# Performance work log

Hardware: AMD Instinct MI355X
Metric: run time of the kernel (lower is better)

The kernel has to match this reference:

```python
import jax, jax.numpy as jnp
import numpy as np

N = 50000      # nodes
E = 800000     # edges
D_IN = 128
D_H = 256
D_OUT = 128
EPS = 1e-5
SLOPE = 0.01   # LeakyReLU negative_slope


def setup_inputs() -> dict:
    key = jax.random.key(0)
    ks = jax.random.split(key, 24)
    inp = {}
    inp["x"] = jax.random.normal(ks[0], (N, D_IN), dtype=jnp.float32)
    inp["edge_index"] = jax.random.randint(ks[1], (2, E), 0, N, dtype=jnp.int32)
    dims = [(D_IN, D_H), (D_H, D_H), (D_H, D_H), (D_H, D_OUT)]
    for i, (di, do) in enumerate(dims, start=1):
        inp[f"W{i}"] = jax.random.normal(ks[4 * i - 2], (di, do), dtype=jnp.float32) / np.float32(np.sqrt(di))
        inp[f"b{i}"] = jnp.zeros((do,), dtype=jnp.float32)
        inp[f"g{i}"] = 1.0 + 0.1 * jax.random.normal(ks[4 * i - 1], (do,), dtype=jnp.float32)   # BN gamma
        inp[f"be{i}"] = 0.1 * jax.random.normal(ks[4 * i], (do,), dtype=jnp.float32)            # BN beta
    inp["ln_g"] = 1.0 + 0.1 * jax.random.normal(ks[18], (D_OUT,), dtype=jnp.float32)
    inp["ln_b"] = 0.1 * jax.random.normal(ks[19], (D_OUT,), dtype=jnp.float32)
    return inp


def _gcn_conv(x, W, b, src, dst, nisq):
    # PyG GCNConv: linear first, then sym-normalized aggregation with self-loops.
    xl = x @ W                                   # [N, do]
    coef = (nisq[src] * nisq[dst])[:, None]      # [E, 1]
    msg = xl[src] * coef                         # [E, do] gather
    agg = jax.ops.segment_sum(msg, dst, num_segments=N)  # scatter-add
    # self-loop contribution: deg^{-1/2}_i * deg^{-1/2}_i * xl_i
    return agg + xl * (nisq * nisq)[:, None] + b


def _bn(x, g, b):
    # BatchNorm1d, training-mode batch statistics (biased variance)
    m = jnp.mean(x, axis=0)
    v = jnp.var(x, axis=0)
    return (x - m) * jax.lax.rsqrt(v + EPS) * g + b


def _lrelu(x):
    return jnp.where(x >= 0, x, SLOPE * x)


def _layer_norm(x, g, b):
    m = jnp.mean(x, axis=-1, keepdims=True)
    v = jnp.var(x, axis=-1, keepdims=True)
    return (x - m) * jax.lax.rsqrt(v + EPS) * g + b


def reference(x, edge_index, W1, b1, g1, be1, W2, b2, g2, be2, W3, b3, g3, be3, W4, b4, g4, be4, ln_g, ln_b):
    src = edge_index[0]
    dst = edge_index[1]
    # degrees with self-loops (computed once, shared by all 4 convs)
    deg = jax.ops.segment_sum(jnp.ones((E,), dtype=x.dtype), dst, num_segments=N) + 1.0
    nisq = jax.lax.rsqrt(deg)  # deg >= 1 so safe

    identity = x  # input_dim == output_dim -> residual_fc is Identity
    h = _lrelu(_bn(_gcn_conv(x, W1, b1, src, dst, nisq), g1, be1))   # dropout = identity (eval)
    h = _lrelu(_bn(_gcn_conv(h, W2, b2, src, dst, nisq), g2, be2))
    h = _lrelu(_bn(_gcn_conv(h, W3, b3, src, dst, nisq), g3, be3))
    h = _gcn_conv(h, W4, b4, src, dst, nisq)
    h = h + identity
    return _layer_norm(_bn(h, g4, be4), ln_g, ln_b)
```

## Files before the change

### kernel.cpp

```cpp
#include <hip/hip_runtime.h>

#define N_NODES 50000
#define NPAD 50176
#define N_EDGES 800000
#define EPS_C 1e-5f
#define SLOPE_C 0.01f

typedef __attribute__((ext_vector_type(8))) short short8v;
typedef __attribute__((ext_vector_type(4))) float f32x4;

__device__ __forceinline__ unsigned short f2bf(float f) {
  unsigned u = __float_as_uint(f);
  u += 0x7fffu + ((u >> 16) & 1u);
  return (unsigned short)(u >> 16);
}
__device__ __forceinline__ unsigned packbf(float a, float b) {
  return (unsigned)f2bf(a) | ((unsigned)f2bf(b) << 16);
}
__device__ __forceinline__ float bflo(unsigned u) { return __uint_as_float(u << 16); }
__device__ __forceinline__ float bfhi(unsigned u) { return __uint_as_float(u & 0xffff0000u); }

__device__ __forceinline__ void gload16(const unsigned short* g, unsigned short* l) {
  __builtin_amdgcn_global_load_lds(
      (const __attribute__((address_space(1))) unsigned int*)g,
      (__attribute__((address_space(3))) unsigned int*)l, 16, 0, 0);
}

__global__ void wcast_all_kernel(const float* __restrict__ W1, const float* __restrict__ W2,
                                 const float* __restrict__ W3, const float* __restrict__ W4,
                                 unsigned short* __restrict__ Wt1, unsigned short* __restrict__ Wt2,
                                 unsigned short* __restrict__ Wt3, unsigned short* __restrict__ Wt4) {
  const int y = blockIdx.y;
  const int idx = blockIdx.x * 256 + threadIdx.x;
  const float* W;
  unsigned short* Wt;
  int K, mshift, mmask, total;
  switch (y) {
    case 0: W = W1; Wt = Wt1; K = 128; mshift = 8; mmask = 255; total = 32768; break;
    case 1: W = W2; Wt = Wt2; K = 256; mshift = 8; mmask = 255; total = 65536; break;
    case 2: W = W3; Wt = Wt3; K = 256; mshift = 8; mmask = 255; total = 65536; break;
    default: W = W4; Wt = Wt4; K = 256; mshift = 7; mmask = 127; total = 32768; break;
  }
  if (idx >= total) return;
  const int k = idx >> mshift;
  const int m = idx & mmask;
  Wt[(size_t)m * K + k] = f2bf(W[idx]);
}

template <int MODE, int KC>
__global__ __launch_bounds__(256) void gemm2_kernel(
    const unsigned short* __restrict__ A, const unsigned short* __restrict__ Wt,
    const float* __restrict__ bias, unsigned short* __restrict__ Yb,
    float* __restrict__ colsum, float* __restrict__ colsumsq, int M) {
  __shared__ __align__(16) unsigned short Bs[64][KC];
  __shared__ __align__(16) unsigned short As[128][64];
  __shared__ float sred[2][64][2];
  const int tid = threadIdx.x;
  const int lane = tid & 63;
  const int wave = tid >> 6;
  const int wr = wave >> 1, wc = wave & 1;
  const int row0 = blockIdx.x * 128;
  const int col0 = blockIdx.y * 64;
  const int l15 = lane & 15;
  const int lhi = lane >> 4;

  constexpr int CPR = KC / 8;
  constexpr int BITER = 64 * CPR / 256;
#pragma unroll
  for (int c = 0; c < BITER; ++c) {
    const int ch = c * 256 + tid;
    const int rb = ch / CPR;
    const int cb = ch % CPR;
    const short8v v =
        *reinterpret_cast<const short8v*>(&Wt[(size_t)(col0 + rb) * KC + cb * 8]);
    *reinterpret_cast<short8v*>(&Bs[rb][(cb ^ (rb & 7)) * 8]) = v;
  }

  f32x4 acc[4][2];
#pragma unroll
  for (int i = 0; i < 4; ++i)
#pragma unroll
    for (int j = 0; j < 2; ++j) acc[i][j] = (f32x4){0.f, 0.f, 0.f, 0.f};

  for (int k0 = 0; k0 < KC; k0 += 64) {
    __syncthreads();
#pragma unroll
    for (int c = 0; c < 4; ++c) {
      const int chunk = (c * 4 + wave) * 64 + lane;
      const int r = chunk >> 3;
      const int cksrc = (chunk & 7) ^ (r & 7);
      gload16(&A[(size_t)(row0 + r) * KC + k0 + cksrc * 8], &As[0][0] + chunk * 8);
    }
    __syncthreads();
    short8v bfr[2][2];
#pragma unroll
    for (int nr = 0; nr < 2; ++nr)
#pragma unroll
      for (int h = 0; h < 2; ++h) {
        const int rowb = wc * 32 + nr * 16 + l15;
        const int chb = (k0 >> 3) + h * 4 + lhi;
        bfr[nr][h] = *reinterpret_cast<const short8v*>(&Bs[rowb][(chb ^ (rowb & 7)) * 8]);
      }
#pragma unroll
    for (int mr = 0; mr < 4; ++mr) {
#pragma unroll
      for (int h = 0; h < 2; ++h) {
        const int rowa = wr * 64 + mr * 16 + l15;
        const int cha = (h * 4 + lhi) ^ (rowa & 7);
        const short8v af = *reinterpret_cast<const short8v*>(&As[rowa][cha * 8]);
#pragma unroll
        for (int nr = 0; nr < 2; ++nr)
          acc[mr][nr] = __builtin_amdgcn_mfma_f32_16x16x32_bf16(
              af, bfr[nr][h], acc[mr][nr], 0, 0, 0);
      }
    }
  }
  float bcol[2] = {0.f, 0.f};
  if constexpr (MODE == 1) {
#pragma unroll
    for (int nr = 0; nr < 2; ++nr) bcol[nr] = bias[col0 + wc * 32 + nr * 16 + l15];
  }
  float s_c[2] = {0.f, 0.f}, q_c[2] = {0.f, 0.f};
#pragma unroll
  for (int mr = 0; mr < 4; ++mr) {
#pragma unroll
    for (int r = 0; r < 4; ++r) {
      const int grow = row0 + wr * 64 + mr * 16 + lhi * 4 + r;
#pragma unroll
      for (int nr = 0; nr < 2; ++nr) {
        const int gcol = col0 + wc * 32 + nr * 16 + l15;
        const float v = acc[mr][nr][r] + bcol[nr];
        Yb[(size_t)grow * M + gcol] = f2bf(v);
        if constexpr (MODE == 1) {
          if (grow < N_NODES) {
            s_c[nr] += v;
            q_c[nr] += v * v;
          }
        }
      }
    }
  }
  if constexpr (MODE == 1) {
#pragma unroll
    for (int nr = 0; nr < 2; ++nr) {
      float s = s_c[nr], q = q_c[nr];
      s += __shfl_xor(s, 16, 64); q += __shfl_xor(q, 16, 64);
      s += __shfl_xor(s, 32, 64); q += __shfl_xor(q, 32, 64);
      if (lhi == 0) {
        const int cl = wc * 32 + nr * 16 + l15;
        sred[0][cl][wr] = s;
        sred[1][cl][wr] = q;
      }
    }
    __syncthreads();
    if (tid < 128) {
      const int which = tid >> 6;
      const int cl = tid & 63;
      const float tot = sred[which][cl][0] + sred[which][cl][1];
      float* dstp = which ? colsumsq : colsum;
      atomicAdd(&dstp[col0 + cl], tot);
    }
  }
}

__global__ void hist_kernel(const int* __restrict__ dst, int* __restrict__ hist, int E) {
  const int e = blockIdx.x * 256 + threadIdx.x;
  if (e < E) atomicAdd(&hist[dst[e]], 1);
}

__global__ __launch_bounds__(1024) void scan1_kernel(
    const int* __restrict__ hist, int* __restrict__ off, int* __restrict__ partial,
    float* __restrict__ nisq, int n) {
  __shared__ int tmp[1024];
  const int tid = threadIdx.x;
  const int i = blockIdx.x * 1024 + tid;
  const int v = (i < n) ? hist[i] : 0;
  tmp[tid] = v;
  __syncthreads();
  int x = v;
  for (int o = 1; o < 1024; o <<= 1) {
    const int y = (tid >= o) ? tmp[tid - o] : 0;
    __syncthreads();
    x += y;
    tmp[tid] = x;
    __syncthreads();
  }
  if (i < n) {
    off[i] = x - v;
    nisq[i] = rsqrtf((float)v + 1.0f);
  }
  if (tid == 1023) partial[blockIdx.x] = x;
}

__global__ __launch_bounds__(64) void scan2_kernel(
    const int* __restrict__ partial, int* __restrict__ partialoff,
    int* __restrict__ offN, int nb) {
  const int tid = threadIdx.x;
  const int v = (tid < nb) ? partial[tid] : 0;
  int x = v;
  for (int o = 1; o < 64; o <<= 1) {
    const int y = __shfl_up(x, o, 64);
    if (tid >= o) x += y;
  }
  if (tid < nb) partialoff[tid] = x - v;
  if (tid == 63) *offN = x;
}

__global__ void scan3_kernel(int* __restrict__ off, int* __restrict__ cursor,
                             const int* __restrict__ partialoff, int n) {
  const int i = blockIdx.x * 256 + threadIdx.x;
  if (i < n) {
    const int o = off[i] + partialoff[i >> 10];
    off[i] = o;
    cursor[i] = o;
  }
}

__global__ void scatter_kernel(const int* __restrict__ src, const int* __restrict__ dst,
                               int* __restrict__ cursor, int* __restrict__ esorted, int E) {
  const int e = blockIdx.x * 256 + threadIdx.x;
  if (e < E) {
    const int p = atomicAdd(&cursor[dst[e]], 1);
    esorted[p] = src[e];
  }
}

__global__ void scale_cast_kernel(const float* __restrict__ x,
                                  const float* __restrict__ nisq,
                                  unsigned short* __restrict__ xs) {
  const int idx = blockIdx.x * 256 + threadIdx.x;
  if (idx >= N_NODES * 32) return;
  const int row = idx >> 5;
  const int c = (idx & 31) * 4;
  const float s = nisq[row];
  const float4 v = *reinterpret_cast<const float4*>(&x[(size_t)row * 128 + c]);
  ushort4 o;
  o.x = f2bf(v.x * s); o.y = f2bf(v.y * s);
  o.z = f2bf(v.z * s); o.w = f2bf(v.w * s);
  *reinterpret_cast<ushort4*>(&xs[(size_t)row * 128 + c]) = o;
}

template <int DO, bool ADD_BIAS, bool HAS_RES, bool OUT_BF16>
__global__ __launch_bounds__(256) void aggregate4_kernel(
    const unsigned short* __restrict__ Y, const int* __restrict__ segoff,
    const int* __restrict__ esorted, const float* __restrict__ nisq,
    const float* __restrict__ bias, const float* __restrict__ resid,
    void* __restrict__ Tv) {
  constexpr int V2 = DO / 32;
  const int wave = threadIdx.x >> 6;
  const int lane = threadIdx.x & 63;
  const int half = lane >> 5;
  const int l31 = lane & 31;
  const int n = blockIdx.x * 4 + wave;
  const int colbase = l31 * V2;
  if (n >= N_NODES) {
    if (half == 0) {
      if constexpr (OUT_BF16) {
        unsigned short* tr = (unsigned short*)Tv + (size_t)n * DO + colbase;
        if constexpr (V2 == 8) *reinterpret_cast<uint4*>(tr) = (uint4){0, 0, 0, 0};
        else *reinterpret_cast<uint2*>(tr) = (uint2){0, 0};
      } else {
        float* tr = (float*)Tv + (size_t)n * DO + colbase;
        if constexpr (V2 == 8) {
          *reinterpret_cast<float4*>(tr) = (float4){0.f, 0.f, 0.f, 0.f};
          *reinterpret_cast<float4*>(tr + 4) = (float4){0.f, 0.f, 0.f, 0.f};
        } else {
          *reinterpret_cast<float4*>(tr) = (float4){0.f, 0.f, 0.f, 0.f};
        }
      }
    }
    return;
  }
  const unsigned short* Yc = Y + colbase;
  float a0[V2], a1[V2];
#pragma unroll
  for (int i = 0; i < V2; ++i) { a0[i] = 0.f; a1[i] = 0.f; }
  const int s = segoff[n];
  const int e = segoff[n + 1];

  if constexpr (V2 == 8) {
    auto acc8 = [&](float* a, const uint4 v) {
      a[0] += bflo(v.x); a[1] += bfhi(v.x);
      a[2] += bflo(v.y); a[3] += bfhi(v.y);
      a[4] += bflo(v.z); a[5] += bfhi(v.z);
      a[6] += bflo(v.w); a[7] += bfhi(v.w);
    };
    int j = s + half;
    for (; j + 2 < e; j += 4) {
      const int i0 = esorted[j];
      const int i1 = esorted[j + 2];
      const uint4 v0 = *reinterpret_cast<const uint4*>(Yc + (size_t)i0 * DO);
      const uint4 v1 = *reinterpret_cast<const uint4*>(Yc + (size_t)i1 * DO);
      acc8(a0, v0); acc8(a1, v1);
    }
    if (j < e) acc8(a0, *reinterpret_cast<const uint4*>(Yc + (size_t)esorted[j] * DO));
    if (half == 0) acc8(a1, *reinterpret_cast<const uint4*>(Yc + (size_t)n * DO));
  } else {
    auto acc4 = [&](float* a, const uint2 v) {
      a[0] += bflo(v.x); a[1] += bfhi(v.x);
      a[2] += bflo(v.y); a[3] += bfhi(v.y);
    };
    int j = s + half;
    for (; j + 2 < e; j += 4) {
      const int i0 = esorted[j];
      const int i1 = esorted[j + 2];
      const uint2 v0 = *reinterpret_cast<const uint2*>(Yc + (size_t)i0 * DO);
      const uint2 v1 = *reinterpret_cast<const uint2*>(Yc + (size_t)i1 * DO);
      acc4(a0, v0); acc4(a1, v1);
    }
    if (j < e) acc4(a0, *reinterpret_cast<const uint2*>(Yc + (size_t)esorted[j] * DO));
    if (half == 0) acc4(a1, *reinterpret_cast<const uint2*>(Yc + (size_t)n * DO));
  }

  const float sc = nisq[n];
  float vals[V2];
#pragma unroll
  for (int i = 0; i < V2; ++i) {
    float t = a0[i] + a1[i];
    t += __shfl_xor(t, 32, 64);
    t *= sc;
    if (half == 0) {
      if (ADD_BIAS) t += bias[colbase + i];
      if (HAS_RES) t += resid[(size_t)n * DO + colbase + i];
    }
    vals[i] = t;
  }
  if (half == 0) {
    if constexpr (OUT_BF16) {
      unsigned short* tr = (unsigned short*)Tv + (size_t)n * DO + colbase;
      if constexpr (V2 == 8) {
        uint4 o;
        o.x = packbf(vals[0], vals[1]); o.y = packbf(vals[2], vals[3]);
        o.z = packbf(vals[4], vals[5]); o.w = packbf(vals[6], vals[7]);
        *reinterpret_cast<uint4*>(tr) = o;
      } else {
        uint2 o;
        o.x = packbf(vals[0], vals[1]); o.y = packbf(vals[2], vals[3]);
        *reinterpret_cast<uint2*>(tr) = o;
      }
    } else {
      float* tr = (float*)Tv + (size_t)n * DO + colbase;
      if constexpr (V2 == 8) {
        float4 o0 = {vals[0], vals[1], vals[2], vals[3]};
        float4 o1 = {vals[4], vals[5], vals[6], vals[7]};
        *reinterpret_cast<float4*>(tr) = o0;
        *reinterpret_cast<float4*>(tr + 4) = o1;
      } else {
        float4 o = {vals[0], vals[1], vals[2], vals[3]};
        *reinterpret_cast<float4*>(tr) = o;
      }
    }
  }
}

__global__ void stats_kernel(const float* __restrict__ T, float* __restrict__ colsum,
                             float* __restrict__ colsumsq, int n, int rowsPerBlock) {
  const int c = threadIdx.x;
  const int DO = blockDim.x;
  const int r0 = blockIdx.x * rowsPerBlock;
  int r1 = r0 + rowsPerBlock;
  if (r1 > n) r1 = n;
  float s = 0.f, q = 0.f;
  for (int r = r0; r < r1; ++r) {
    const float v = T[(size_t)r * DO + c];
    s += v;
    q += v * v;
  }
  atomicAdd(&colsum[c], s);
  atomicAdd(&colsumsq[c], q);
}

__global__ void bn_lrelu_nisq_kernel(const unsigned short* __restrict__ Tb,
                                     const float* __restrict__ colsum,
                                     const float* __restrict__ colsumsq,
                                     const float* __restrict__ g, const float* __restrict__ be,
                                     const float* __restrict__ nisq,
                                     unsigned short* __restrict__ outb,
                                     size_t total8, float invN) {
  const size_t idx = (size_t)blockIdx.x * 256 + threadIdx.x;
  if (idx >= total8) return;
  const int row = (int)(idx >> 5);
  if (row >= N_NODES) {
    *reinterpret_cast<uint4*>(&outb[idx * 8]) = (uint4){0, 0, 0, 0};
    return;
  }
  const unsigned c = ((unsigned)idx & 31u) * 8;
  const float sc = nisq[row];
  uint4 v = *reinterpret_cast<const uint4*>(&Tb[idx * 8]);
  float z[8] = {bflo(v.x), bfhi(v.x), bflo(v.y), bfhi(v.y),
                bflo(v.z), bfhi(v.z), bflo(v.w), bfhi(v.w)};
  const float4 cs0 = *reinterpret_cast<const float4*>(&colsum[c]);
  const float4 cs1 = *reinterpret_cast<const float4*>(&colsum[c + 4]);
  const float4 cq0 = *reinterpret_cast<const float4*>(&colsumsq[c]);
  const float4 cq1 = *reinterpret_cast<const float4*>(&colsumsq[c + 4]);
  const float4 gv0 = *reinterpret_cast<const float4*>(&g[c]);
  const float4 gv1 = *reinterpret_cast<const float4*>(&g[c + 4]);
  const float4 bv0 = *reinterpret_cast<const float4*>(&be[c]);
  const float4 bv1 = *reinterpret_cast<const float4*>(&be[c + 4]);
  const float css[8] = {cs0.x, cs0.y, cs0.z, cs0.w, cs1.x, cs1.y, cs1.z, cs1.w};
  const float cqq[8] = {cq0.x, cq0.y, cq0.z, cq0.w, cq1.x, cq1.y, cq1.z, cq1.w};
  const float ggg[8] = {gv0.x, gv0.y, gv0.z, gv0.w, gv1.x, gv1.y, gv1.z, gv1.w};
  const float bbb[8] = {bv0.x, bv0.y, bv0.z, bv0.w, bv1.x, bv1.y, bv1.z, bv1.w};
#pragma unroll
  for (int k = 0; k < 8; ++k) {
    const float m = css[k] * invN;
    const float rs = rsqrtf(cqq[k] * invN - m * m + EPS_C);
    float zz = (z[k] - m) * rs * ggg[k] + bbb[k];
    zz = (zz >= 0.f) ? zz : SLOPE_C * zz;
    z[k] = zz * sc;
  }
  v.x = packbf(z[0], z[1]); v.y = packbf(z[2], z[3]);
  v.z = packbf(z[4], z[5]); v.w = packbf(z[6], z[7]);
  *reinterpret_cast<uint4*>(&outb[idx * 8]) = v;
}

__global__ __launch_bounds__(256) void bn_ln_kernel(
    const float* __restrict__ T, const float* __restrict__ colsum,
    const float* __restrict__ colsumsq, const float* __restrict__ g,
    const float* __restrict__ be, const float* __restrict__ lng,
    const float* __restrict__ lnb, float* __restrict__ out, float invN) {
  const int wave = threadIdx.x >> 6;
  const int lane = threadIdx.x & 63;
  const int n = blockIdx.x * 4 + wave;
  if (n >= N_NODES) return;
  const int c = lane * 2;
  const float2 t = *reinterpret_cast<const float2*>(&T[(size_t)n * 128 + c]);
  float z[2];
#pragma unroll
  for (int k = 0; k < 2; ++k) {
    const float m = colsum[c + k] * invN;
    const float v = colsumsq[c + k] * invN - m * m;
    const float tv = (k == 0) ? t.x : t.y;
    z[k] = (tv - m) * rsqrtf(v + EPS_C) * g[c + k] + be[c + k];
  }
  float s = z[0] + z[1];
  float q = z[0] * z[0] + z[1] * z[1];
  for (int o = 32; o > 0; o >>= 1) {
    s += __shfl_xor(s, o, 64);
    q += __shfl_xor(q, o, 64);
  }
  const float mean = s * (1.f / 128.f);
  const float var = q * (1.f / 128.f) - mean * mean;
  const float rs = rsqrtf(var + EPS_C);
  float2 o2;
  o2.x = (z[0] - mean) * rs * lng[c] + lnb[c];
  o2.y = (z[1] - mean) * rs * lng[c + 1] + lnb[c + 1];
  *reinterpret_cast<float2*>(&out[(size_t)n * 128 + c]) = o2;
}

extern "C" void kernel_launch(void* const* d_in, const int* in_sizes, int n_in,
                              void* d_out, int out_size, void* d_ws, size_t ws_size,
                              hipStream_t stream) {
  const float* x = (const float*)d_in[0];
  const int* ei = (const int*)d_in[1];
  const int* srcp = ei;
  const int* dstp = ei + N_EDGES;
  const float* W1 = (const float*)d_in[2];
  const float* b1 = (const float*)d_in[3];
  const float* g1 = (const float*)d_in[4];
  const float* be1 = (const float*)d_in[5];
  const float* W2 = (const float*)d_in[6];
  const float* b2 = (const float*)d_in[7];
  const float* g2 = (const float*)d_in[8];
  const float* be2 = (const float*)d_in[9];
  const float* W3 = (const float*)d_in[10];
  const float* b3 = (const float*)d_in[11];
  const float* g3 = (const float*)d_in[12];
  const float* be3 = (const float*)d_in[13];
  const float* W4 = (const float*)d_in[14];
  const float* b4 = (const float*)d_in[15];
  const float* g4 = (const float*)d_in[16];
  const float* be4 = (const float*)d_in[17];
  const float* lng = (const float*)d_in[18];
  const float* lnb = (const float*)d_in[19];
  float* out = (float*)d_out;

  char* ws = (char*)d_ws;
  size_t off_b = 0;
  auto alloc = [&](size_t bytes) -> void* {
    void* p = (void*)(ws + off_b);
    off_b += (bytes + 255) & ~(size_t)255;
    return p;
  };
  int* hist = (int*)alloc((size_t)N_NODES * 4);
  float* cs1 = (float*)alloc(256 * 4);
  float* cq1 = (float*)alloc(256 * 4);
  float* cs2 = (float*)alloc(256 * 4);
  float* cq2 = (float*)alloc(256 * 4);
  float* cs3 = (float*)alloc(256 * 4);
  float* cq3 = (float*)alloc(256 * 4);
  float* cs4 = (float*)alloc(256 * 4);
  float* cq4 = (float*)alloc(256 * 4);
  const size_t zero_bytes = off_b;
  int* segoff = (int*)alloc((size_t)(N_NODES + 1) * 4);
  int* cursor = (int*)alloc((size_t)N_NODES * 4);
  float* nisq = (float*)alloc((size_t)N_NODES * 4);
  int* esorted = (int*)alloc((size_t)N_EDGES * 4);
  int* partial = (int*)alloc(64 * 4);
  int* partialoff = (int*)alloc(64 * 4);
  unsigned short* Wt1 = (unsigned short*)alloc((size_t)256 * 128 * 2);
  unsigned short* Wt2 = (unsigned short*)alloc((size_t)256 * 256 * 2);
  unsigned short* Wt3 = (unsigned short*)alloc((size_t)256 * 256 * 2);
  unsigned short* Wt4 = (unsigned short*)alloc((size_t)128 * 256 * 2);
  unsigned short* tblA = (unsigned short*)alloc((size_t)NPAD * 256 * 2);
  unsigned short* tblB = (unsigned short*)alloc((size_t)NPAD * 256 * 2);
  unsigned short* S = (unsigned short*)alloc((size_t)NPAD * 256 * 2);
  unsigned short* Tb = (unsigned short*)alloc((size_t)NPAD * 256 * 2);
  float* Tf = (float*)alloc((size_t)NPAD * 128 * 4);

  const float invN = 1.0f / (float)N_NODES;
  const int egrid = (N_EDGES + 255) / 256;
  const int ngrid = (N_NODES + 255) / 256;
  const int aggrid = NPAD / 4;
  const int statgrid = (N_NODES + 127) / 128;
  const int nb = (N_NODES + 1023) / 1024;
  const dim3 mgrid256(NPAD / 128, 4);
  const dim3 mgrid128(NPAD / 128, 2);
  const unsigned bngrid = (unsigned)(((size_t)NPAD * 32 + 255) / 256);

  hipMemsetAsync(hist, 0, zero_bytes, stream);

  hist_kernel<<<egrid, 256, 0, stream>>>(dstp, hist, N_EDGES);
  scan1_kernel<<<nb, 1024, 0, stream>>>(hist, segoff, partial, nisq, N_NODES);
  scan2_kernel<<<1, 64, 0, stream>>>(partial, partialoff, &segoff[N_NODES], nb);
  scan3_kernel<<<ngrid, 256, 0, stream>>>(segoff, cursor, partialoff, N_NODES);
  scatter_kernel<<<egrid, 256, 0, stream>>>(srcp, dstp, cursor, esorted, N_EDGES);

  wcast_all_kernel<<<dim3(256, 4), 256, 0, stream>>>(W1, W2, W3, W4, Wt1, Wt2, Wt3, Wt4);

  scale_cast_kernel<<<(N_NODES * 32 + 255) / 256, 256, 0, stream>>>(x, nisq, tblA);
  aggregate4_kernel<128, false, false, true><<<aggrid, 256, 0, stream>>>(
      tblA, segoff, esorted, nisq, nullptr, nullptr, S);
  gemm2_kernel<1, 128><<<mgrid256, 256, 0, stream>>>(S, Wt1, b1, Tb, cs1, cq1, 256);
  bn_lrelu_nisq_kernel<<<bngrid, 256, 0, stream>>>(Tb, cs1, cq1, g1, be1, nisq,
                                                   tblB, (size_t)NPAD * 32, invN);

  aggregate4_kernel<256, false, false, true><<<aggrid, 256, 0, stream>>>(
      tblB, segoff, esorted, nisq, nullptr, nullptr, S);
  gemm2_kernel<1, 256><<<mgrid256, 256, 0, stream>>>(S, Wt2, b2, Tb, cs2, cq2, 256);
  bn_lrelu_nisq_kernel<<<bngrid, 256, 0, stream>>>(Tb, cs2, cq2, g2, be2, nisq,
                                                   tblA, (size_t)NPAD * 32, invN);

  aggregate4_kernel<256, false, false, true><<<aggrid, 256, 0, stream>>>(
      tblA, segoff, esorted, nisq, nullptr, nullptr, S);
  gemm2_kernel<1, 256><<<mgrid256, 256, 0, stream>>>(S, Wt3, b3, Tb, cs3, cq3, 256);
  bn_lrelu_nisq_kernel<<<bngrid, 256, 0, stream>>>(Tb, cs3, cq3, g3, be3, nisq,
                                                   tblB, (size_t)NPAD * 32, invN);

  gemm2_kernel<0, 256><<<mgrid128, 256, 0, stream>>>(tblB, Wt4, nullptr, S, nullptr, nullptr, 128);
  aggregate4_kernel<128, true, true, false><<<aggrid, 256, 0, stream>>>(
      S, segoff, esorted, nisq, b4, x, Tf);
  stats_kernel<<<statgrid, 128, 0, stream>>>(Tf, cs4, cq4, N_NODES, 128);
  bn_ln_kernel<<<(N_NODES + 3) / 4, 256, 0, stream>>>(Tf, cs4, cq4, g4, be4, lng, lnb, out, invN);
}
```

Measured before the change: 504.2 us.

## Double-buffer GEMM tiles with async LDS loads and store final layer in bf16

New measurement: 519.6 us. 3.1% more time.

```diff
diff --git a/kernel.cpp b/kernel.cpp
--- a/kernel.cpp
+++ b/kernel.cpp
@@ -48,12 +48,12 @@
 }
 
 template <int MODE, int KC>
-__global__ __launch_bounds__(256) void gemm2_kernel(
+__global__ __launch_bounds__(256) void gemm3_kernel(
     const unsigned short* __restrict__ A, const unsigned short* __restrict__ Wt,
     const float* __restrict__ bias, unsigned short* __restrict__ Yb,
     float* __restrict__ colsum, float* __restrict__ colsumsq, int M) {
-  __shared__ __align__(16) unsigned short Bs[64][KC];
-  __shared__ __align__(16) unsigned short As[128][64];
+  __shared__ __align__(16) unsigned short As[2][128][64];
+  __shared__ __align__(16) unsigned short Bs[2][64][64];
   __shared__ float sred[2][64][2];
   const int tid = threadIdx.x;
   const int lane = tid & 63;
@@ -64,42 +64,44 @@
   const int l15 = lane & 15;
   const int lhi = lane >> 4;
 
-  constexpr int CPR = KC / 8;
-  constexpr int BITER = 64 * CPR / 256;
-#pragma unroll
-  for (int c = 0; c < BITER; ++c) {
-    const int ch = c * 256 + tid;
-    const int rb = ch / CPR;
-    const int cb = ch % CPR;
-    const short8v v =
-        *reinterpret_cast<const short8v*>(&Wt[(size_t)(col0 + rb) * KC + cb * 8]);
-    *reinterpret_cast<short8v*>(&Bs[rb][(cb ^ (rb & 7)) * 8]) = v;
-  }
-
-  f32x4 acc[4][2];
-#pragma unroll
-  for (int i = 0; i < 4; ++i)
-#pragma unroll
-    for (int j = 0; j < 2; ++j) acc[i][j] = (f32x4){0.f, 0.f, 0.f, 0.f};
-
-  for (int k0 = 0; k0 < KC; k0 += 64) {
-    __syncthreads();
+  auto stage = [&](int b, int k0) {
 #pragma unroll
     for (int c = 0; c < 4; ++c) {
       const int chunk = (c * 4 + wave) * 64 + lane;
       const int r = chunk >> 3;
-      const int cksrc = (chunk & 7) ^ (r & 7);
-      gload16(&A[(size_t)(row0 + r) * KC + k0 + cksrc * 8], &As[0][0] + chunk * 8);
-    }
-    __syncthreads();
+      const int ck = (chunk & 7) ^ (r & 7);
+      gload16(&A[(size_t)(row0 + r) * KC + k0 + ck * 8], &As[b][0][0] + chunk * 8);
+    }
+#pragma unroll
+    for (int c = 0; c < 2; ++c) {
+      const int chunk = (c * 4 + wave) * 64 + lane;
+      const int rb = chunk >> 3;
+      const int cb = (chunk & 7) ^ (rb & 7);
+      gload16(&Wt[(size_t)(col0 + rb) * KC + k0 + cb * 8], &Bs[b][0][0] + chunk * 8);
+    }
+  };
+
+  f32x4 acc[4][2];
+#pragma unroll
+  for (int i = 0; i < 4; ++i)
+#pragma unroll
+    for (int j = 0; j < 2; ++j) acc[i][j] = (f32x4){0.f, 0.f, 0.f, 0.f};
+
+  constexpr int NK = KC / 64;
+  stage(0, 0);
+  __syncthreads();
+#pragma unroll
+  for (int step = 0; step < NK; ++step) {
+    if (step + 1 < NK) stage((step + 1) & 1, (step + 1) * 64);
+    const int b = step & 1;
     short8v bfr[2][2];
 #pragma unroll
     for (int nr = 0; nr < 2; ++nr)
 #pragma unroll
       for (int h = 0; h < 2; ++h) {
         const int rowb = wc * 32 + nr * 16 + l15;
-        const int chb = (k0 >> 3) + h * 4 + lhi;
-        bfr[nr][h] = *reinterpret_cast<const short8v*>(&Bs[rowb][(chb ^ (rowb & 7)) * 8]);
+        const int chb = (h * 4 + lhi) ^ (rowb & 7);
+        bfr[nr][h] = *reinterpret_cast<const short8v*>(&Bs[b][rowb][chb * 8]);
       }
 #pragma unroll
     for (int mr = 0; mr < 4; ++mr) {
@@ -107,13 +109,14 @@
       for (int h = 0; h < 2; ++h) {
         const int rowa = wr * 64 + mr * 16 + l15;
         const int cha = (h * 4 + lhi) ^ (rowa & 7);
-        const short8v af = *reinterpret_cast<const short8v*>(&As[rowa][cha * 8]);
+        const short8v af = *reinterpret_cast<const short8v*>(&As[b][rowa][cha * 8]);
 #pragma unroll
         for (int nr = 0; nr < 2; ++nr)
           acc[mr][nr] = __builtin_amdgcn_mfma_f32_16x16x32_bf16(
               af, bfr[nr][h], acc[mr][nr], 0, 0, 0);
       }
     }
+    __syncthreads();
   }
   float bcol[2] = {0.f, 0.f};
   if constexpr (MODE == 1) {
@@ -353,21 +356,27 @@
   }
 }
 
-__global__ void stats_kernel(const float* __restrict__ T, float* __restrict__ colsum,
-                             float* __restrict__ colsumsq, int n, int rowsPerBlock) {
-  const int c = threadIdx.x;
-  const int DO = blockDim.x;
+__global__ void stats_bf16_kernel(const unsigned short* __restrict__ T,
+                                  float* __restrict__ colsum, float* __restrict__ colsumsq,
+                                  int n, int rowsPerBlock) {
+  const int t = threadIdx.x;
+  const int c2 = t & 63;
+  const int rh = t >> 6;
   const int r0 = blockIdx.x * rowsPerBlock;
   int r1 = r0 + rowsPerBlock;
   if (r1 > n) r1 = n;
-  float s = 0.f, q = 0.f;
-  for (int r = r0; r < r1; ++r) {
-    const float v = T[(size_t)r * DO + c];
-    s += v;
-    q += v * v;
-  }
-  atomicAdd(&colsum[c], s);
-  atomicAdd(&colsumsq[c], q);
+  const unsigned* T32 = (const unsigned*)T;
+  float s0 = 0.f, q0 = 0.f, s1 = 0.f, q1 = 0.f;
+  for (int r = r0 + rh; r < r1; r += 2) {
+    const unsigned v = T32[(size_t)r * 64 + c2];
+    const float a = bflo(v), b = bfhi(v);
+    s0 += a; q0 += a * a;
+    s1 += b; q1 += b * b;
+  }
+  atomicAdd(&colsum[c2 * 2], s0);
+  atomicAdd(&colsumsq[c2 * 2], q0);
+  atomicAdd(&colsum[c2 * 2 + 1], s1);
+  atomicAdd(&colsumsq[c2 * 2 + 1], q1);
 }
 
 __global__ void bn_lrelu_nisq_kernel(const unsigned short* __restrict__ Tb,
@@ -415,7 +424,7 @@
 }
 
 __global__ __launch_bounds__(256) void bn_ln_kernel(
-    const float* __restrict__ T, const float* __restrict__ colsum,
+    const unsigned short* __restrict__ T, const float* __restrict__ colsum,
     const float* __restrict__ colsumsq, const float* __restrict__ g,
     const float* __restrict__ be, const float* __restrict__ lng,
     const float* __restrict__ lnb, float* __restrict__ out, float invN) {
@@ -424,14 +433,15 @@
   const int n = blockIdx.x * 4 + wave;
   if (n >= N_NODES) return;
   const int c = lane * 2;
-  const float2 t = *reinterpret_cast<const float2*>(&T[(size_t)n * 128 + c]);
+  const unsigned tv = *reinterpret_cast<const unsigned*>(&T[(size_t)n * 128 + c]);
+  const float t0 = bflo(tv), t1 = bfhi(tv);
   float z[2];
 #pragma unroll
   for (int k = 0; k < 2; ++k) {
     const float m = colsum[c + k] * invN;
     const float v = colsumsq[c + k] * invN - m * m;
-    const float tv = (k == 0) ? t.x : t.y;
-    z[k] = (tv - m) * rsqrtf(v + EPS_C) * g[c + k] + be[c + k];
+    const float tvv = (k == 0) ? t0 : t1;
+    z[k] = (tvv - m) * rsqrtf(v + EPS_C) * g[c + k] + be[c + k];
   }
   float s = z[0] + z[1];
   float q = z[0] * z[0] + z[1] * z[1];
@@ -506,7 +516,6 @@
   unsigned short* tblB = (unsigned short*)alloc((size_t)NPAD * 256 * 2);
   unsigned short* S = (unsigned short*)alloc((size_t)NPAD * 256 * 2);
   unsigned short* Tb = (unsigned short*)alloc((size_t)NPAD * 256 * 2);
-  float* Tf = (float*)alloc((size_t)NPAD * 128 * 4);
 
   const float invN = 1.0f / (float)N_NODES;
   const int egrid = (N_EDGES + 255) / 256;
@@ -531,25 +540,25 @@
   scale_cast_kernel<<<(N_NODES * 32 + 255) / 256, 256, 0, stream>>>(x, nisq, tblA);
   aggregate4_kernel<128, false, false, true><<<aggrid, 256, 0, stream>>>(
       tblA, segoff, esorted, nisq, nullptr, nullptr, S);
-  gemm2_kernel<1, 128><<<mgrid256, 256, 0, stream>>>(S, Wt1, b1, Tb, cs1, cq1, 256);
+  gemm3_kernel<1, 128><<<mgrid256, 256, 0, stream>>>(S, Wt1, b1, Tb, cs1, cq1, 256);
   bn_lrelu_nisq_kernel<<<bngrid, 256, 0, stream>>>(Tb, cs1, cq1, g1, be1, nisq,
                                                    tblB, (size_t)NPAD * 32, invN);
 
   aggregate4_kernel<256, false, false, true><<<aggrid, 256, 0, stream>>>(
       tblB, segoff, esorted, nisq, nullptr, nullptr, S);
-  gemm2_kernel<1, 256><<<mgrid256, 256, 0, stream>>>(S, Wt2, b2, Tb, cs2, cq2, 256);
+  gemm3_kernel<1, 256><<<mgrid256, 256, 0, stream>>>(S, Wt2, b2, Tb, cs2, cq2, 256);
   bn_lrelu_nisq_kernel<<<bngrid, 256, 0, stream>>>(Tb, cs2, cq2, g2, be2, nisq,
                                                    tblA, (size_t)NPAD * 32, invN);
 
   aggregate4_kernel<256, false, false, true><<<aggrid, 256, 0, stream>>>(
       tblA, segoff, esorted, nisq, nullptr, nullptr, S);
-  gemm2_kernel<1, 256><<<mgrid256, 256, 0, stream>>>(S, Wt3, b3, Tb, cs3, cq3, 256);
+  gemm3_kernel<1, 256><<<mgrid256, 256, 0, stream>>>(S, Wt3, b3, Tb, cs3, cq3, 256);
   bn_lrelu_nisq_kernel<<<bngrid, 256, 0, stream>>>(Tb, cs3, cq3, g3, be3, nisq,
                                                    tblB, (size_t)NPAD * 32, invN);
 
-  gemm2_kernel<0, 256><<<mgrid128, 256, 0, stream>>>(tblB, Wt4, nullptr, S, nullptr, nullptr, 128);
-  aggregate4_kernel<128, true, true, false><<<aggrid, 256, 0, stream>>>(
-      S, segoff, esorted, nisq, b4, x, Tf);
-  stats_kernel<<<statgrid, 128, 0, stream>>>(Tf, cs4, cq4, N_NODES, 128);
-  bn_ln_kernel<<<(N_NODES + 3) / 4, 256, 0, stream>>>(Tf, cs4, cq4, g4, be4, lng, lnb, out, invN);
-}
+  gemm3_kernel<0, 256><<<mgrid128, 256, 0, stream>>>(tblB, Wt4, nullptr, S, nullptr, nullptr, 128);
+  aggregate4_kernel<128, true, true, true><<<aggrid, 256, 0, stream>>>(
+      S, segoff, esorted, nisq, b4, x, Tb);
+  stats_bf16_kernel<<<statgrid, 128, 0, stream>>>(Tb, cs4, cq4, N_NODES, 128);
+  bn_ln_kernel<<<(N_NODES + 3) / 4, 256, 0, stream>>>(Tb, cs4, cq4, g4, be4, lng, lnb, out, invN);
+}
```
